# Kernel optimization log

Hardware: AMD Instinct MI355X
Metric: run time of the kernel (lower is better)

Reference implementation:

```python
import jax, jax.numpy as jnp
import numpy as np

N = 4096        # batch size (rows)
K = 4           # instances per class -> num_instances in the torch code
D = 256         # embedding dim
MARGIN = 0.5
SAMPLE_KEY = jax.random.key(42)  # fixed key: deterministic stand-in for torch.multinomial


def setup_inputs() -> dict:
    key = jax.random.key(0)
    x = jax.random.normal(key, (N, D), dtype=jnp.float32)
    # L2-normalize like typical metric-learning embeddings so sims are in [-1, 1]
    inputs = x / jnp.linalg.norm(x, axis=1, keepdims=True)
    targets = (jnp.arange(N) // K).astype(jnp.int32)  # P*K batch: equal-size classes
    return {"inputs": inputs, "targets": targets}


def reference(inputs, targets):
    n = inputs.shape[0]
    km1 = K - 1                 # positives per row
    n_neg = n - K               # negatives per row

    sim = inputs @ inputs.T                                   # [n, n]
    same = targets[:, None] == targets[None, :]
    eye = jnp.eye(n, dtype=bool)
    pos_mask = same & ~eye
    neg_mask = ~same

    # masked_select + per-row sort: masked entries -> +inf, ascending sort,
    # keep first count entries (counts are uniform across rows)
    pos_sorted = jnp.sort(jnp.where(pos_mask, sim, jnp.inf), axis=1)[:, :km1]   # [n, K-1]
    neg_sorted = jnp.sort(jnp.where(neg_mask, sim, jnp.inf), axis=1)[:, :n_neg] # [n, n-K]

    pos_d = jnp.mean(pos_sorted)
    neg_d = jnp.mean(neg_sorted)

    # GaussDistribution per row over negatives
    neg_mean = jnp.mean(neg_sorted, axis=1, keepdims=True)
    neg_std = jnp.sqrt(jnp.mean((neg_sorted - neg_mean) ** 2, axis=1, keepdims=True))
    # NOTE: the original uses exp(+(x-mu)^2 / (2 sigma^2)) (no minus sign) -- faithful
    logprob = (neg_sorted - neg_mean) ** 2 / (2.0 * neg_std ** 2)               # [n, n-K]

    # multinomial without replacement ~ Gumbel top-k on log-weights
    gumbel = -jnp.log(-jnp.log(
        jax.random.uniform(SAMPLE_KEY, logprob.shape, minval=1e-20, maxval=1.0)))
    _, neg_idx = jax.lax.top_k(logprob + gumbel, km1)                            # [n, K-1]
    neg_pair = jnp.take_along_axis(neg_sorted, neg_idx, axis=1)                  # [n, K-1]

    pos_loss = jnp.mean(jnp.log1p(jnp.exp(-2.0 * (pos_sorted - MARGIN))), axis=1)
    neg_loss = 0.04 * jnp.mean(jnp.log1p(jnp.exp(50.0 * (neg_pair - MARGIN))), axis=1)
    loss = jnp.sum(pos_loss + neg_loss) / n

    # prec: fraction of rows where hardest positive > hardest sampled negative + 0.05
    c = jnp.sum(pos_sorted[:, -1] > jnp.max(neg_pair, axis=1) + 0.05)
    prec = c.astype(jnp.float32) / n

    return loss, prec, pos_d, neg_d
```

## Files before the change

kernel.cpp:

```cpp
#include <hip/hip_runtime.h>
#include <hip/hip_bf16.h>
#include <cstdint>
#include <cfloat>
#include <math.h>

#define NN 4096
#define DD 256
#define NNEG 4092
#define MARGIN 0.5f
#define NB 3584
#define NW (NB / 2)

__device__ __forceinline__ uint32_t rotl32(uint32_t x, int r) {
  return (x << r) | (x >> (32 - r));
}

__device__ __forceinline__ void threefry2x32_42(uint32_t x0, uint32_t x1,
                                                uint32_t& o0, uint32_t& o1) {
  const uint32_t k0 = 0u, k1 = 42u;
  const uint32_t k2 = k0 ^ k1 ^ 0x1BD11BDAu;
  x0 += k0; x1 += k1;
#define TF_R(r) { x0 += x1; x1 = rotl32(x1, r); x1 ^= x0; }
  TF_R(13) TF_R(15) TF_R(26) TF_R(6)
  x0 += k1; x1 += k2 + 1u;
  TF_R(17) TF_R(29) TF_R(16) TF_R(24)
  x0 += k2; x1 += k0 + 2u;
  TF_R(13) TF_R(15) TF_R(26) TF_R(6)
  x0 += k0; x1 += k1 + 3u;
  TF_R(17) TF_R(29) TF_R(16) TF_R(24)
  x0 += k1; x1 += k2 + 4u;
  TF_R(13) TF_R(15) TF_R(26) TF_R(6)
  x0 += k2; x1 += k0 + 5u;
#undef TF_R
  o0 = x0; o1 = x1;
}

__device__ __forceinline__ float gumbel_at(uint32_t f) {
  uint32_t o0, o1;
  threefry2x32_42(0u, f, o0, o1);
  uint32_t bits = o0 ^ o1;
  uint32_t fb = (bits >> 9) | 0x3F800000u;
  float fl = __uint_as_float(fb) - 1.0f;
  float u = fmaxf(1e-20f, fl + 1e-20f);
  return -logf(-logf(u));
}

__device__ __forceinline__ int bucket_of(float v) {
  return (int)fminf(fmaxf((v + 0.5f) * (float)NB, 0.0f), (float)(NB - 1));
}

#define BT 128
#define NT (NN / BT)
#define BK 32
#define LDSS 36

__global__ __launch_bounds__(256) void gemm_sim(const float* __restrict__ X,
                                                float* __restrict__ S) {
  __shared__ float As[BT * LDSS];
  __shared__ float Bs[BT * LDSS];
  const int tid = threadIdx.x;
  const int tx = tid & 15, ty = tid >> 4;

  int b = blockIdx.x, bi = 0;
  while (b >= NT - bi) { b -= NT - bi; bi++; }
  const int bj = bi + b;
  const int rowBase = bi * BT, colBase = bj * BT;

  float acc[8][8] = {};
  for (int kb = 0; kb < DD; kb += BK) {
#pragma unroll
    for (int it = 0; it < 4; ++it) {
      int idx = tid + 256 * it;
      int r = idx >> 3, c4 = idx & 7;
      float4 av = *(const float4*)(X + (size_t)(rowBase + r) * DD + kb + c4 * 4);
      float4 bv = *(const float4*)(X + (size_t)(colBase + r) * DD + kb + c4 * 4);
      *(float4*)(As + r * LDSS + c4 * 4) = av;
      *(float4*)(Bs + r * LDSS + c4 * 4) = bv;
    }
    __syncthreads();
    for (int k = 0; k < BK; k += 4) {
      float4 a[8], bfr[8];
#pragma unroll
      for (int i = 0; i < 8; ++i) a[i] = *(const float4*)(As + (ty + 16 * i) * LDSS + k);
#pragma unroll
      for (int j = 0; j < 8; ++j) bfr[j] = *(const float4*)(Bs + (tx + 16 * j) * LDSS + k);
#pragma unroll
      for (int i = 0; i < 8; ++i)
#pragma unroll
        for (int j = 0; j < 8; ++j) {
          acc[i][j] += a[i].x * bfr[j].x;
          acc[i][j] += a[i].y * bfr[j].y;
          acc[i][j] += a[i].z * bfr[j].z;
          acc[i][j] += a[i].w * bfr[j].w;
        }
    }
    __syncthreads();
  }
#pragma unroll
  for (int i = 0; i < 8; ++i)
#pragma unroll
    for (int j = 0; j < 8; ++j)
      S[(size_t)(rowBase + ty + 16 * i) * NN + colBase + tx + 16 * j] = acc[i][j];
  if (bi != bj) {
#pragma unroll
    for (int i = 0; i < 8; ++i)
#pragma unroll
      for (int j = 0; j < 8; ++j)
        S[(size_t)(colBase + tx + 16 * j) * NN + rowBase + ty + 16 * i] = acc[i][j];
  }
}

#define INSERT3(sc, v)                                              \
  if ((sc) > s2) {                                                  \
    if ((sc) > s1) {                                                \
      s2 = s1; v2 = v1;                                             \
      if ((sc) > s0) { s1 = s0; v1 = v0; s0 = (sc); v0 = (v); }     \
      else           { s1 = (sc); v1 = (v); }                       \
    } else { s2 = (sc); v2 = (v); }                                 \
  }

__global__ __launch_bounds__(256) void row_kernel(const float* __restrict__ S,
                                                  float* __restrict__ acc) {
  __shared__ uint32_t histw[NW];
  __shared__ uint32_t offsw[NW];
  __shared__ float sval[NN];
  __shared__ float sh[48];
  __shared__ uint32_t wtot[4];

  const int row = blockIdx.x;
  const int tid = threadIdx.x;
  const int lane = tid & 63, wid = tid >> 6;

#pragma unroll
  for (int i = 0; i < 7; ++i) histw[tid + 256 * i] = 0u;

  const float4* src = (const float4*)(S + (size_t)row * NN);
  const int pslot = row >> 2;
  float vv[16];
#pragma unroll
  for (int it = 0; it < 4; ++it) {
    int slot = tid + 256 * it;
    float4 t4 = src[slot];
    if (slot == pslot) {
      sh[16] = t4.x; sh[17] = t4.y; sh[18] = t4.z; sh[19] = t4.w;
      t4.x = INFINITY; t4.y = INFINITY; t4.z = INFINITY; t4.w = INFINITY;
    }
    vv[4 * it + 0] = t4.x; vv[4 * it + 1] = t4.y;
    vv[4 * it + 2] = t4.z; vv[4 * it + 3] = t4.w;
  }

  float s = 0.0f;
#pragma unroll
  for (int e = 0; e < 16; ++e) if (vv[e] < 1e30f) s += vv[e];
#pragma unroll
  for (int off = 32; off > 0; off >>= 1) s += __shfl_down(s, off, 64);
  if (lane == 0) sh[5 + wid] = s;
  __syncthreads();

#pragma unroll
  for (int e = 0; e < 16; ++e) {
    int b = bucket_of(vv[e]);
    atomicAdd(&histw[b >> 1], 1u << ((b & 1) << 4));
  }
  if (tid == 0) {
    int self = row & 3;
    float p[3]; int m = 0;
#pragma unroll
    for (int c = 0; c < 4; ++c)
      if (c != self) p[m++] = sh[16 + c];
    float t;
    if (p[0] > p[1]) { t = p[0]; p[0] = p[1]; p[1] = t; }
    if (p[1] > p[2]) { t = p[1]; p[1] = p[2]; p[2] = t; }
    if (p[0] > p[1]) { t = p[0]; p[0] = p[1]; p[1] = t; }
    sh[0] = p[0]; sh[1] = p[1]; sh[2] = p[2];
    float tot = sh[5] + sh[6] + sh[7] + sh[8];
    sh[9] = tot;
    sh[3] = tot / (float)NNEG;
  }
  __syncthreads();

  uint32_t hw[7];
  uint32_t s14 = 0;
#pragma unroll
  for (int j = 0; j < 7; ++j) {
    hw[j] = histw[7 * tid + j];
    s14 += (hw[j] & 0xFFFFu) + (hw[j] >> 16);
  }
  uint32_t inc = s14;
#pragma unroll
  for (int off = 1; off < 64; off <<= 1) {
    uint32_t n = __shfl_up(inc, (unsigned)off, 64);
    if (lane >= off) inc += n;
  }
  if (lane == 63) wtot[wid] = inc;

  const float mu = sh[3];
  float q = 0.0f;
#pragma unroll
  for (int e = 0; e < 16; ++e)
    if (vv[e] < 1e30f) { float d = vv[e] - mu; q += d * d; }
#pragma unroll
  for (int off = 32; off > 0; off >>= 1) q += __shfl_down(q, off, 64);
  if (lane == 0) sh[10 + wid] = q;
  __syncthreads();

  uint32_t wbase = 0;
  for (int w = 0; w < wid; ++w) wbase += wtot[w];
  uint32_t run = wbase + inc - s14;
#pragma unroll
  for (int j = 0; j < 7; ++j) {
    uint32_t lo = run; run += hw[j] & 0xFFFFu;
    uint32_t hi = run; run += hw[j] >> 16;
    offsw[7 * tid + j] = lo | (hi << 16);
  }
  if (tid == 0) {
    float var = (sh[10] + sh[11] + sh[12] + sh[13]) / (float)NNEG;
    float sd = sqrtf(var);
    sh[4] = 1.0f / (2.0f * sd * sd);
  }
  __syncthreads();

#pragma unroll
  for (int e = 0; e < 16; ++e) {
    int b = bucket_of(vv[e]);
    uint32_t old = atomicAdd(&offsw[b >> 1], 1u << ((b & 1) << 4));
    uint32_t sl = (old >> ((b & 1) << 4)) & 0xFFFFu;
    sval[sl] = vv[e];
  }
  __syncthreads();

  const float inv2s2 = sh[4];
  const uint32_t fbase = (uint32_t)row * (uint32_t)NNEG;
  float s0 = -FLT_MAX, s1 = -FLT_MAX, s2 = -FLT_MAX;
  float v0 = 0.0f, v1 = 0.0f, v2 = 0.0f;
#pragma unroll 1
  for (int it = 0; it < 16; ++it) {
    int sl = tid + 256 * it;
    float v = sval[sl];
    if (v < 1e30f) {
      int b = bucket_of(v);
      uint32_t sh16 = (uint32_t)((b & 1) << 4);
      uint32_t end = (offsw[b >> 1] >> sh16) & 0xFFFFu;
      uint32_t cntb = (histw[b >> 1] >> sh16) & 0xFFFFu;
      uint32_t st = end - cntb;
      int cnt = (int)st;
      for (uint32_t u = st; u < end; ++u) {
        float w = sval[u];
        cnt += (w < v || (w == v && (int)u < sl)) ? 1 : 0;
      }
      float d = v - mu;
      float sc = d * d * inv2s2 + gumbel_at(fbase + (uint32_t)cnt);
      INSERT3(sc, v)
    }
  }

#pragma unroll
  for (int dlt = 1; dlt < 64; dlt <<= 1) {
    float t0 = __shfl_xor(s0, dlt, 64), u0 = __shfl_xor(v0, dlt, 64);
    float t1 = __shfl_xor(s1, dlt, 64), u1 = __shfl_xor(v1, dlt, 64);
    float t2 = __shfl_xor(s2, dlt, 64), u2 = __shfl_xor(v2, dlt, 64);
    INSERT3(t0, u0)
    INSERT3(t1, u1)
    INSERT3(t2, u2)
  }
  if (lane == 0) {
    int b0 = 24 + wid * 6;
    sh[b0 + 0] = s0; sh[b0 + 1] = v0;
    sh[b0 + 2] = s1; sh[b0 + 3] = v1;
    sh[b0 + 4] = s2; sh[b0 + 5] = v2;
  }
  __syncthreads();

  if (tid == 0) {
    float g0 = -FLT_MAX, g1 = -FLT_MAX, g2 = -FLT_MAX;
    float w0 = 0.0f, w1 = 0.0f, w2 = 0.0f;
    {
      float s0 = g0, s1 = g1, s2 = g2, v0 = w0, v1 = w1, v2 = w2;
#pragma unroll
      for (int i = 0; i < 12; ++i) {
        float sc = sh[24 + 2 * i], v = sh[24 + 2 * i + 1];
        INSERT3(sc, v)
      }
      g0 = s0; g1 = s1; g2 = s2; w0 = v0; w1 = v1; w2 = v2;
    }
    float negmax = fmaxf(w0, fmaxf(w1, w2));
    float neg_loss = 0.04f * (log1pf(expf(50.0f * (w0 - MARGIN))) +
                              log1pf(expf(50.0f * (w1 - MARGIN))) +
                              log1pf(expf(50.0f * (w2 - MARGIN)))) / 3.0f;
    float p0 = sh[0], p1 = sh[1], p2 = sh[2];
    float pos_loss = (log1pf(expf(-2.0f * (p0 - MARGIN))) +
                      log1pf(expf(-2.0f * (p1 - MARGIN))) +
                      log1pf(expf(-2.0f * (p2 - MARGIN)))) / 3.0f;
    atomicAdd(&acc[0], pos_loss + neg_loss);
    if (p2 > negmax + 0.05f) atomicAdd(&acc[1], 1.0f);
    atomicAdd(&acc[2], p0 + p1 + p2);
    atomicAdd(&acc[3], sh[9]);
  }
}

__global__ void finalize(const float* __restrict__ acc, float* out) {
  if (threadIdx.x == 0 && blockIdx.x == 0) {
    out[0] = acc[0] / 4096.0f;
    out[1] = acc[1] / 4096.0f;
    out[2] = acc[2] / (4096.0f * 3.0f);
    out[3] = acc[3] / (4096.0f * 4092.0f);
  }
}

extern "C" void kernel_launch(void* const* d_in, const int* in_sizes, int n_in,
                              void* d_out, int out_size, void* d_ws, size_t ws_size,
                              hipStream_t stream) {
  (void)in_sizes; (void)n_in; (void)out_size; (void)ws_size;
  const float* X = (const float*)d_in[0];
  float* S = (float*)d_ws;
  float* acc = (float*)((char*)d_ws + (size_t)NN * NN * 4);
  hipMemsetAsync(acc, 0, 4 * sizeof(float), stream);
  gemm_sim<<<NT * (NT + 1) / 2, 256, 0, stream>>>(X, S);
  row_kernel<<<NN, 256, 0, stream>>>(S, acc);
  finalize<<<1, 64, 0, stream>>>(acc, (float*)d_out);
}
```

Measured before the change: 368.2 us.

## Double-buffer GEMM LDS tiles, merge histogram/offset arrays, use fast log

The similarity GEMM now keeps two LDS tile buffers per operand and prefetches the next K-slice into registers while computing on the current one, so one barrier per iteration is dropped and global-load latency is overlapped. The row kernel reuses the histogram array for the post-scatter bucket offsets and derives bucket start and end from neighbouring end offsets, which removes one shared array and one LDS read. The Gumbel noise uses __logf instead of logf, which is cheaper but less accurate and could shift the sampled top-k. Double buffering also raises LDS and register use in the GEMM, which may lower occupancy.

```diff
diff --git a/kernel.cpp b/kernel.cpp
--- a/kernel.cpp
+++ b/kernel.cpp
@@ -42,7 +42,7 @@
   uint32_t fb = (bits >> 9) | 0x3F800000u;
   float fl = __uint_as_float(fb) - 1.0f;
   float u = fmaxf(1e-20f, fl + 1e-20f);
-  return -logf(-logf(u));
+  return -__logf(-__logf(u));
 }
 
 __device__ __forceinline__ int bucket_of(float v) {
@@ -56,8 +56,8 @@
 
 __global__ __launch_bounds__(256) void gemm_sim(const float* __restrict__ X,
                                                 float* __restrict__ S) {
-  __shared__ float As[BT * LDSS];
-  __shared__ float Bs[BT * LDSS];
+  __shared__ float As[2][BT * LDSS];
+  __shared__ float Bs[2][BT * LDSS];
   const int tid = threadIdx.x;
   const int tx = tid & 15, ty = tid >> 4;
 
@@ -66,24 +66,43 @@
   const int bj = bi + b;
   const int rowBase = bi * BT, colBase = bj * BT;
 
+  int r_[4], c_[4];
+  float4 av[4], bv[4];
+#pragma unroll
+  for (int it = 0; it < 4; ++it) {
+    int idx = tid + 256 * it;
+    r_[it] = idx >> 3;
+    c_[it] = (idx & 7) * 4;
+    av[it] = *(const float4*)(X + (size_t)(rowBase + r_[it]) * DD + c_[it]);
+    bv[it] = *(const float4*)(X + (size_t)(colBase + r_[it]) * DD + c_[it]);
+  }
+#pragma unroll
+  for (int it = 0; it < 4; ++it) {
+    *(float4*)(&As[0][r_[it] * LDSS + c_[it]]) = av[it];
+    *(float4*)(&Bs[0][r_[it] * LDSS + c_[it]]) = bv[it];
+  }
+  __syncthreads();
+
   float acc[8][8] = {};
-  for (int kb = 0; kb < DD; kb += BK) {
-#pragma unroll
-    for (int it = 0; it < 4; ++it) {
-      int idx = tid + 256 * it;
-      int r = idx >> 3, c4 = idx & 7;
-      float4 av = *(const float4*)(X + (size_t)(rowBase + r) * DD + kb + c4 * 4);
-      float4 bv = *(const float4*)(X + (size_t)(colBase + r) * DD + kb + c4 * 4);
-      *(float4*)(As + r * LDSS + c4 * 4) = av;
-      *(float4*)(Bs + r * LDSS + c4 * 4) = bv;
-    }
-    __syncthreads();
+  int cur = 0;
+  for (int kbi = 0; kbi < DD / BK; ++kbi) {
+    if (kbi + 1 < DD / BK) {
+      int kb = (kbi + 1) * BK;
+#pragma unroll
+      for (int it = 0; it < 4; ++it) {
+        av[it] = *(const float4*)(X + (size_t)(rowBase + r_[it]) * DD + kb + c_[it]);
+        bv[it] = *(const float4*)(X + (size_t)(colBase + r_[it]) * DD + kb + c_[it]);
+      }
+    }
+    const float* Ac = As[cur];
+    const float* Bc = Bs[cur];
+#pragma unroll
     for (int k = 0; k < BK; k += 4) {
       float4 a[8], bfr[8];
 #pragma unroll
-      for (int i = 0; i < 8; ++i) a[i] = *(const float4*)(As + (ty + 16 * i) * LDSS + k);
-#pragma unroll
-      for (int j = 0; j < 8; ++j) bfr[j] = *(const float4*)(Bs + (tx + 16 * j) * LDSS + k);
+      for (int i = 0; i < 8; ++i) a[i] = *(const float4*)(Ac + (ty + 16 * i) * LDSS + k);
+#pragma unroll
+      for (int j = 0; j < 8; ++j) bfr[j] = *(const float4*)(Bc + (tx + 16 * j) * LDSS + k);
 #pragma unroll
       for (int i = 0; i < 8; ++i)
 #pragma unroll
@@ -94,7 +113,16 @@
           acc[i][j] += a[i].w * bfr[j].w;
         }
     }
-    __syncthreads();
+    if (kbi + 1 < DD / BK) {
+      int nxt = cur ^ 1;
+#pragma unroll
+      for (int it = 0; it < 4; ++it) {
+        *(float4*)(&As[nxt][r_[it] * LDSS + c_[it]]) = av[it];
+        *(float4*)(&Bs[nxt][r_[it] * LDSS + c_[it]]) = bv[it];
+      }
+      __syncthreads();
+      cur = nxt;
+    }
   }
 #pragma unroll
   for (int i = 0; i < 8; ++i)
@@ -122,7 +150,6 @@
 __global__ __launch_bounds__(256) void row_kernel(const float* __restrict__ S,
                                                   float* __restrict__ acc) {
   __shared__ uint32_t histw[NW];
-  __shared__ uint32_t offsw[NW];
   __shared__ float sval[NN];
   __shared__ float sh[48];
   __shared__ uint32_t wtot[4];
@@ -211,7 +238,7 @@
   for (int j = 0; j < 7; ++j) {
     uint32_t lo = run; run += hw[j] & 0xFFFFu;
     uint32_t hi = run; run += hw[j] >> 16;
-    offsw[7 * tid + j] = lo | (hi << 16);
+    histw[7 * tid + j] = lo | (hi << 16);
   }
   if (tid == 0) {
     float var = (sh[10] + sh[11] + sh[12] + sh[13]) / (float)NNEG;
@@ -223,7 +250,7 @@
 #pragma unroll
   for (int e = 0; e < 16; ++e) {
     int b = bucket_of(vv[e]);
-    uint32_t old = atomicAdd(&offsw[b >> 1], 1u << ((b & 1) << 4));
+    uint32_t old = atomicAdd(&histw[b >> 1], 1u << ((b & 1) << 4));
     uint32_t sl = (old >> ((b & 1) << 4)) & 0xFFFFu;
     sval[sl] = vv[e];
   }
@@ -239,14 +266,17 @@
     float v = sval[sl];
     if (v < 1e30f) {
       int b = bucket_of(v);
-      uint32_t sh16 = (uint32_t)((b & 1) << 4);
-      uint32_t end = (offsw[b >> 1] >> sh16) & 0xFFFFu;
-      uint32_t cntb = (histw[b >> 1] >> sh16) & 0xFFFFu;
-      uint32_t st = end - cntb;
+      uint32_t w = histw[b >> 1];
+      uint32_t end, st;
+      if (b & 1) { end = w >> 16; st = w & 0xFFFFu; }
+      else {
+        end = w & 0xFFFFu;
+        st = (b == 0) ? 0u : (histw[(b >> 1) - 1] >> 16);
+      }
       int cnt = (int)st;
       for (uint32_t u = st; u < end; ++u) {
-        float w = sval[u];
-        cnt += (w < v || (w == v && (int)u < sl)) ? 1 : 0;
+        float wv = sval[u];
+        cnt += (wv < v || (wv == v && (int)u < sl)) ? 1 : 0;
       }
       float d = v - mu;
       float sc = d * d * inv2s2 + gumbel_at(fbase + (uint32_t)cnt);
```

After: 622.0 us. 68.9% more time.
